# Optimization experiments

Measured on AMD Instinct MI355X. Metric: run time of the kernel, lower is better.

The kernel has to match this reference:

```python
import jax, jax.numpy as jnp
import numpy as np

B, C, T, H, F, KS = 8, 512, 1024, 8, 2048, 3
K = C // H            # head channels = 64
ROPE_D = K // 2       # RoPE rotates half the head channels = 32
EPS = 1e-4


def setup_inputs() -> dict:
    key = jax.random.key(0)
    ks = jax.random.split(key, 12)
    s = 1.0 / np.sqrt(C)
    sf = 1.0 / np.sqrt(F)
    return {
        "x": jax.random.normal(ks[0], (B, C, T), jnp.float32),
        "x_mask": jnp.ones((B, 1, T), jnp.float32),
        "attn_mask": jnp.ones((B, 1, T, T), jnp.float32),
        "wq": jax.random.normal(ks[1], (C, C), jnp.float32) * s,
        "bq": jnp.zeros((C,), jnp.float32),
        "wk": jax.random.normal(ks[2], (C, C), jnp.float32) * s,
        "bk": jnp.zeros((C,), jnp.float32),
        "wv": jax.random.normal(ks[3], (C, C), jnp.float32) * s,
        "bv": jnp.zeros((C,), jnp.float32),
        "wo": jax.random.normal(ks[4], (C, C), jnp.float32) * s,
        "bo": jnp.zeros((C,), jnp.float32),
        "w1": jax.random.normal(ks[5], (F, C, KS), jnp.float32) * s,
        "b1": jnp.zeros((F,), jnp.float32),
        "w2": jax.random.normal(ks[6], (C, F, KS), jnp.float32) * sf,
        "b2": jnp.zeros((C,), jnp.float32),
        "g1": jnp.ones((C,), jnp.float32),
        "be1": jnp.zeros((C,), jnp.float32),
        "g2": jnp.ones((C,), jnp.float32),
        "be2": jnp.zeros((C,), jnp.float32),
    }


def _rope(x):
    # x: (B, H, T, K); rotate first ROPE_D channels, pass the rest through.
    t = x.shape[2]
    theta = 1.0 / (10000.0 ** (jnp.arange(0, ROPE_D, 2, dtype=jnp.float32) / ROPE_D))
    idx = jnp.arange(t, dtype=jnp.float32)[:, None] * theta[None, :]  # (T, d/2)
    idx2 = jnp.concatenate([idx, idx], axis=-1)                       # (T, d)
    cos, sin = jnp.cos(idx2), jnp.sin(idx2)                           # broadcast over B,H
    xr, xp = x[..., :ROPE_D], x[..., ROPE_D:]
    h = ROPE_D // 2
    neg = jnp.concatenate([-xr[..., h:], xr[..., :h]], axis=-1)
    return jnp.concatenate([xr * cos + neg * sin, xp], axis=-1)


def _ln(x, gamma, beta):
    # channel-wise LayerNorm over dim 1 of (B, C, T), eps=1e-4
    mean = jnp.mean(x, axis=1, keepdims=True)
    var = jnp.mean((x - mean) ** 2, axis=1, keepdims=True)
    xn = (x - mean) * jax.lax.rsqrt(var + EPS)
    return xn * gamma[None, :, None] + beta[None, :, None]


def _conv1d(x, w, b):
    # x: (B, Cin, T), w: (Cout, Cin, KS), 'same' padding (KS//2)
    y = jax.lax.conv_general_dilated(
        x, w, window_strides=(1,), padding=[(KS // 2, KS // 2)],
        dimension_numbers=("NCH", "OIH", "NCH"))
    return y + b[None, :, None]


def _forward(x, x_mask, attn_mask, wq, bq, wk, bk, wv, bv, wo, bo,
             w1, b1, w2, b2, g1, be1, g2, be2):
    x = x * x_mask
    # 1x1 conv projections == channel matmuls
    q = jnp.einsum("oc,bct->bot", wq, x) + bq[None, :, None]
    k = jnp.einsum("oc,bct->bot", wk, x) + bk[None, :, None]
    v = jnp.einsum("oc,bct->bot", wv, x) + bv[None, :, None]
    # (B, C, T) -> (B, H, T, K)
    def heads(a):
        return a.reshape(B, H, K, T).transpose(0, 1, 3, 2)
    q, k, v = heads(q), heads(k), heads(v)
    q = _rope(q)
    k = _rope(k)
    scores = jnp.einsum("bhtk,bhsk->bhts", q, k) / jnp.sqrt(jnp.float32(K))
    scores = jnp.where(attn_mask == 0, jnp.float32(-10000.0), scores)
    p = jax.nn.softmax(scores, axis=-1)
    o = jnp.einsum("bhts,bhsk->bhtk", p, v)              # (B,H,T,K)
    o = o.transpose(0, 1, 3, 2).reshape(B, C, T)
    y = jnp.einsum("oc,bct->bot", wo, o) + bo[None, :, None]
    x = _ln(x + y, g1, be1)
    # conv FFN
    h1 = jax.nn.relu(_conv1d(x * x_mask, w1, b1))
    y = _conv1d(h1 * x_mask, w2, b2) * x_mask
    x = _ln(x + y, g2, be2)
    return x


def reference(x, x_mask, attn_mask, wq, bq, wk, bk, wv, bv, wo, bo,
              w1, b1, w2, b2, g1, be1, g2, be2):
    return _forward(x, x_mask, attn_mask, wq, bq, wk, bk, wv, bv, wo, bo,
                    w1, b1, w2, b2, g1, be1, g2, be2)
```

## Files before the change

### kernel.cpp

```cpp
#include <hip/hip_runtime.h>

typedef unsigned short u16;
typedef __attribute__((ext_vector_type(4))) float floatx4;
typedef __attribute__((ext_vector_type(8))) __bf16 bf16x8;
typedef __attribute__((ext_vector_type(4))) unsigned short ushort4v;
typedef __attribute__((ext_vector_type(8))) unsigned short ushort8v;

#define DI __device__ __forceinline__


DI u16 f2bf(float f) {
  union { float f; unsigned u; } v; v.f = f;
  unsigned r = v.u + 0x7fffu + ((v.u >> 16) & 1u);
  return (u16)(r >> 16);
}
DI float bf2f(u16 h) {
  union { unsigned u; float f; } v; v.u = ((unsigned)h) << 16;
  return v.f;
}

#define GLDS(g, l) __builtin_amdgcn_global_load_lds( \
    (const __attribute__((address_space(1))) unsigned int*)(g), \
    (__attribute__((address_space(3))) unsigned int*)(l), 16, 0, 0)

__global__ __launch_bounds__(256, 2) void k_fattn(
    const u16* __restrict__ qb, const u16* __restrict__ kb,
    const u16* __restrict__ vb, const unsigned* __restrict__ mb,
    u16* __restrict__ oT)
{
  __shared__ __align__(16) u16 Ps[4][32 * 64];
  const int tid  = threadIdx.x;
  const int wave = tid >> 6, lane = tid & 63;
  const int lr = lane & 15, kg = lane >> 4;
  const int qt = blockIdx.x, bh = blockIdx.y;
  const int bb = bh >> 3, hh = bh & 7;
  const int wq0 = qt * 128 + wave * 32;
  const float L2E = 1.44269504f;

  const u16* Qp = qb + (size_t)bh * 65536;
  const u16* Kp = kb + (size_t)bh * 65536;
  const u16* Vp = vb + (size_t)bh * 65536;
  u16* Pw = &Ps[wave][0];

  bf16x8 qf[2][2];
#pragma unroll
  for (int i = 0; i < 2; ++i)
#pragma unroll
    for (int h = 0; h < 2; ++h)
      qf[i][h] = *(const bf16x8*)&Qp[(wq0 + i * 16 + lr) * 64 + h * 32 + kg * 8];

  float l_b[2] = {0.f, 0.f};
  floatx4 o_acc[2][4];
#pragma unroll
  for (int i = 0; i < 2; ++i)
#pragma unroll
    for (int j = 0; j < 4; ++j) o_acc[i][j] = (floatx4){0.f, 0.f, 0.f, 0.f};

  bf16x8 kf[4][2], vf[4][2];
#pragma unroll
  for (int a = 0; a < 4; ++a)
#pragma unroll
    for (int h = 0; h < 2; ++h)
      kf[a][h] = *(const bf16x8*)&Kp[(a * 16 + lr) * 64 + h * 32 + kg * 8];

  for (int it = 0; it < 16; ++it) {
    const int s0 = it * 64;
    unsigned mw[2][2];
#pragma unroll
    for (int b = 0; b < 2; ++b) {
      const size_t rw = ((size_t)bb << 15) + ((size_t)(wq0 + b * 16 + lr) << 5) + (s0 >> 5);
      mw[b][0] = mb[rw]; mw[b][1] = mb[rw + 1];
    }
    floatx4 sT[4][2];
    __builtin_amdgcn_s_setprio(1);
#pragma unroll
    for (int a = 0; a < 4; ++a) {
      sT[a][0] = (floatx4){0.f, 0.f, 0.f, 0.f};
      sT[a][1] = (floatx4){0.f, 0.f, 0.f, 0.f};
#pragma unroll
      for (int b = 0; b < 2; ++b)
#pragma unroll
        for (int h = 0; h < 2; ++h)
          sT[a][b] = __builtin_amdgcn_mfma_f32_16x16x32_bf16(kf[a][h], qf[b][h], sT[a][b], 0, 0, 0);
    }
    __builtin_amdgcn_s_setprio(0);
#pragma unroll
    for (int a = 0; a < 4; ++a)
#pragma unroll
      for (int h = 0; h < 2; ++h)
        vf[a][h] = *(const bf16x8*)&Vp[(a * 16 + lr) * 1024 + s0 + h * 32 + kg * 8];
    if (it < 15) {
      const int sn = s0 + 64;
#pragma unroll
      for (int a = 0; a < 4; ++a)
#pragma unroll
        for (int h = 0; h < 2; ++h)
          kf[a][h] = *(const bf16x8*)&Kp[(sn + a * 16 + lr) * 64 + h * 32 + kg * 8];
    }
#pragma unroll
    for (int b = 0; b < 2; ++b) {
      float sum = 0.f;
#pragma unroll
      for (int a = 0; a < 4; ++a)
#pragma unroll
        for (int r = 0; r < 4; ++r) {
          const int sl = a * 16 + kg * 4 + r;
          float sv = sT[a][b][r];
          const unsigned wsel = (sl & 32) ? mw[b][1] : mw[b][0];
          if (!((wsel >> (sl & 31)) & 1u)) sv = -10000.f;
          const float p = exp2f(sv * L2E);
          sT[a][b][r] = p;
          sum += p;
        }
      l_b[b] += sum;
#pragma unroll
      for (int a = 0; a < 4; ++a) {
        ushort4v pk;
#pragma unroll
        for (int r = 0; r < 4; ++r) {
          __bf16 hv = (__bf16)sT[a][b][r];
          pk[r] = *(u16*)&hv;
        }
        const int sl0 = a * 16 + kg * 4;
        *(ushort4v*)&Pw[(b * 16 + lr) * 64 + (sl0 ^ ((lr & 7) << 3))] = pk;
      }
    }
    asm volatile("s_waitcnt lgkmcnt(0)" ::: "memory");
    __builtin_amdgcn_sched_barrier(0);
    bf16x8 pa[2][2];
#pragma unroll
    for (int i = 0; i < 2; ++i)
#pragma unroll
      for (int h = 0; h < 2; ++h)
        pa[i][h] = *(const bf16x8*)&Pw[(i * 16 + lr) * 64 + (((h * 4 + kg) ^ (lr & 7)) << 3)];
    __builtin_amdgcn_s_setprio(1);
#pragma unroll
    for (int jd = 0; jd < 4; ++jd)
#pragma unroll
      for (int i = 0; i < 2; ++i)
#pragma unroll
        for (int h = 0; h < 2; ++h)
          o_acc[i][jd] = __builtin_amdgcn_mfma_f32_16x16x32_bf16(pa[i][h], vf[jd][h], o_acc[i][jd], 0, 0, 0);
    __builtin_amdgcn_s_setprio(0);
  }
#pragma unroll
  for (int i = 0; i < 2; ++i) {
    l_b[i] += __shfl_xor(l_b[i], 16);
    l_b[i] += __shfl_xor(l_b[i], 32);
  }
  float linv[2][4];
#pragma unroll
  for (int i = 0; i < 2; ++i)
#pragma unroll
    for (int r = 0; r < 4; ++r) linv[i][r] = 1.f / __shfl(l_b[i], kg * 4 + r);
#pragma unroll
  for (int i = 0; i < 2; ++i)
#pragma unroll
    for (int jd = 0; jd < 4; ++jd)
#pragma unroll
      for (int r = 0; r < 4; ++r) {
        const int t = wq0 + i * 16 + kg * 4 + r;
        const int c = hh * 64 + jd * 16 + lr;
        oT[((size_t)bb * 1024 + t) * 512 + c] = f2bf(o_acc[i][jd][r] * linv[i][r]);
      }
}

template<int MODE, int BN, int TAPK>
__global__ __launch_bounds__(256) void k_cgemm(
    const u16* __restrict__ A, int lda,
    const u16* __restrict__ Bsrc, int ldb,
    int K,
    u16* __restrict__ o0, u16* __restrict__ o1, u16* __restrict__ o2,
    const float* __restrict__ bias,
    const float* __restrict__ ctab, const float* __restrict__ stab,
    const float* __restrict__ msk)
{
  constexpr int BM = 128;
  constexpr int FN = BN / 32;
  __shared__ __align__(16) u16 As[2 * BM * 32];
  __shared__ __align__(16) u16 Bs[2 * BN * 32];

  const int tid  = threadIdx.x;
  const int wave = tid >> 6, lane = tid & 63;
  const int wm = wave >> 1, wn = wave & 1;
  const int lr = lane & 15, kg = lane >> 4;

  const int nwg = gridDim.x * gridDim.y;
  const int h0  = blockIdx.y * gridDim.x + blockIdx.x;
  const int cpx = nwg >> 3;
  const int tl  = (h0 & 7) * cpx + (h0 >> 3);
  const int bx  = tl % gridDim.x;
  const int by  = tl / gridDim.x;

  const int m0 = bx * BM, n0 = by * BN;
  const int koff = blockIdx.z * K;

  const u16* aP[2][BM / 64];
  const u16* bP[2][BN / 64];
#pragma unroll
  for (int h = 0; h < 2; ++h) {
#pragma unroll
    for (int ch = 0; ch < BM / 64; ++ch) {
      const int idx = ch * 256 + tid;
      const int row = idx >> 2;
      const int kk = (((idx & 3) ^ ((row >> 1) & 3)) << 3);
      aP[h][ch] = A + (size_t)(m0 + row) * lda + koff + h * 32 + kk;
    }
#pragma unroll
    for (int ch = 0; ch < BN / 64; ++ch) {
      const int idx = ch * 256 + tid;
      const int row = idx >> 2;
      const int kk = (((idx & 3) ^ ((row >> 1) & 3)) << 3);
      const int bt = n0 + row;
      size_t rowbase;
      if constexpr (TAPK == 0) {
        rowbase = (size_t)bt * ldb;
      } else {
        const int b = bt >> 10, t = bt & 1023;
        rowbase = ((size_t)(b * 1026 + t)) * TAPK;
      }
      bP[h][ch] = Bsrc + rowbase + koff + h * 32 + kk;
    }
  }

  floatx4 acc[4][FN];
#pragma unroll
  for (int i = 0; i < 4; ++i)
#pragma unroll
    for (int j = 0; j < FN; ++j) acc[i][j] = (floatx4){0.f, 0.f, 0.f, 0.f};

  const int csw = (kg ^ ((lr >> 1) & 3)) * 8;

  for (int k0 = 0; k0 < K; k0 += 64) {
#pragma unroll
    for (int h = 0; h < 2; ++h) {
#pragma unroll
      for (int ch = 0; ch < BM / 64; ++ch)
        GLDS(aP[h][ch] + k0, &As[h * BM * 32 + (ch * 256 + tid) * 8]);
#pragma unroll
      for (int ch = 0; ch < BN / 64; ++ch)
        GLDS(bP[h][ch] + k0, &Bs[h * BN * 32 + (ch * 256 + tid) * 8]);
    }
    __syncthreads();
    bf16x8 af[2][4], bfr[2][FN];
#pragma unroll
    for (int h = 0; h < 2; ++h) {
#pragma unroll
      for (int i = 0; i < 4; ++i)
        af[h][i] = *(const bf16x8*)&As[(h * BM + wm * 64 + i * 16 + lr) * 32 + csw];
#pragma unroll
      for (int j = 0; j < FN; ++j)
        bfr[h][j] = *(const bf16x8*)&Bs[(h * BN + wn * (BN / 2) + j * 16 + lr) * 32 + csw];
    }
#pragma unroll
    for (int h = 0; h < 2; ++h)
#pragma unroll
      for (int i = 0; i < 4; ++i)
#pragma unroll
        for (int j = 0; j < FN; ++j)
          acc[i][j] = __builtin_amdgcn_mfma_f32_16x16x32_bf16(af[h][i], bfr[h][j], acc[i][j], 0, 0, 0);
    __syncthreads();
  }

  const int wrow0 = m0 + wm * 64;
  const int col0  = n0 + wn * (BN / 2);

  if constexpr (MODE == 0) {
    float v[4][FN][4];
#pragma unroll
    for (int i = 0; i < 4; ++i)
#pragma unroll
      for (int j = 0; j < FN; ++j)
#pragma unroll
        for (int r = 0; r < 4; ++r)
          v[i][j][r] = acc[i][j][r] + bias[wrow0 + i * 16 + kg * 4 + r];
    const int sec = wrow0 >> 9;
    const int hh  = (wrow0 & 511) >> 6;
    if (sec < 2) {
      if (sec == 0) {
#pragma unroll
        for (int i = 0; i < 4; ++i)
#pragma unroll
          for (int j = 0; j < FN; ++j)
#pragma unroll
            for (int r = 0; r < 4; ++r) v[i][j][r] *= 0.125f;
      }
#pragma unroll
      for (int j = 0; j < FN; ++j) {
        const int t = (col0 + j * 16 + lr) & 1023;
#pragma unroll
        for (int r = 0; r < 4; ++r) {
          const int a = kg * 4 + r;
          const float cv = ctab[t * 16 + a], sv = stab[t * 16 + a];
          const float a0 = v[0][j][r], a1 = v[1][j][r];
          v[0][j][r] = a0 * cv - a1 * sv;
          v[1][j][r] = a1 * cv + a0 * sv;
        }
      }
      u16* dst = (sec == 0) ? o0 : o1;
#pragma unroll
      for (int i = 0; i < 4; ++i)
#pragma unroll
        for (int j = 0; j < FN; ++j) {
          const int bt = col0 + j * 16 + lr;
          const int b = bt >> 10, t = bt & 1023;
          ushort4v pk;
#pragma unroll
          for (int r = 0; r < 4; ++r) pk[r] = f2bf(v[i][j][r]);
          *(ushort4v*)&dst[(((size_t)b * 8 + hh) * 1024 + t) * 64 + i * 16 + kg * 4] = pk;
        }
    } else {
#pragma unroll
      for (int i = 0; i < 4; ++i)
#pragma unroll
        for (int j = 0; j < FN; ++j) {
          const int bt = col0 + j * 16 + lr;
          const int b = bt >> 10, t = bt & 1023;
#pragma unroll
          for (int r = 0; r < 4; ++r) {
            const int dk = i * 16 + kg * 4 + r;
            o2[(((size_t)b * 8 + hh) * 64 + dk) * 1024 + t] = f2bf(v[i][j][r]);
          }
        }
    }
  } else if constexpr (MODE == 3) {
#pragma unroll
    for (int i = 0; i < 4; ++i)
#pragma unroll
      for (int j = 0; j < FN; ++j) {
        const int bt = col0 + j * 16 + lr;
        const int c0 = wrow0 + i * 16 + kg * 4;
        ushort4v pk;
#pragma unroll
        for (int r = 0; r < 4; ++r) pk[r] = f2bf(acc[i][j][r] + bias[c0 + r]);
        *(ushort4v*)&o0[(size_t)bt * 512 + c0] = pk;
      }
  } else if constexpr (MODE == 4) {
#pragma unroll
    for (int i = 0; i < 4; ++i) {
      const int r0 = wrow0 + i * 16 + kg * 4;
#pragma unroll
      for (int j = 0; j < FN; ++j) {
        const int bt = col0 + j * 16 + lr;
        const int b = bt >> 10, t = bt & 1023;
        const float mv = msk[(size_t)b * 1024 + t];
        ushort4v pk;
#pragma unroll
        for (int r = 0; r < 4; ++r)
          pk[r] = f2bf(fmaxf(acc[i][j][r] + bias[r0 + r], 0.f) * mv);
        *(ushort4v*)&o0[((size_t)(b * 1026 + t + 1)) * 2048 + r0] = pk;
      }
    }
  } else {
    u16* dst = o0 + (size_t)blockIdx.z * 8 * 1024 * 512;
    const bool z0 = (blockIdx.z == 0);
#pragma unroll
    for (int i = 0; i < 4; ++i)
#pragma unroll
      for (int j = 0; j < FN; ++j) {
        const int bt = col0 + j * 16 + lr;
        const int b = bt >> 10, t = bt & 1023;
        const int c0 = wrow0 + i * 16 + kg * 4;
        const float mv = msk[(size_t)b * 1024 + t];
        ushort4v pk;
#pragma unroll
        for (int r = 0; r < 4; ++r) {
          const float bv = z0 ? bias[c0 + r] : 0.f;
          pk[r] = f2bf((acc[i][j][r] + bv) * mv);
        }
        *(ushort4v*)&dst[(size_t)bt * 512 + c0] = pk;
      }
  }
}

__global__ __launch_bounds__(256) void k_prep(
    const float* __restrict__ wq, const float* __restrict__ wk,
    const float* __restrict__ wv, const float* __restrict__ wo,
    const float* __restrict__ w1, const float* __restrict__ w2,
    const float* __restrict__ bq, const float* __restrict__ bk,
    const float* __restrict__ bv, const float* __restrict__ am,
    u16* __restrict__ wqkv, u16* __restrict__ wob,
    u16* __restrict__ w1p, u16* __restrict__ w2p,
    float* __restrict__ bqkv, float* __restrict__ ctab, float* __restrict__ stab,
    unsigned* __restrict__ mbits, u16* __restrict__ x2p, u16* __restrict__ h1p)
{
  const int bid = blockIdx.x;
  if (bid < 4096) {
    const int seg = bid >> 10;
    const int i = (bid & 1023) * 256 + threadIdx.x;
    const float* src = (seg == 0) ? wq : (seg == 1) ? wk : (seg == 2) ? wv : wo;
    u16* dst = (seg < 3) ? (wqkv + (size_t)seg * 512 * 512) : wob;
    dst[i] = f2bf(src[i]);
  } else if (bid < 16384) {
    const int i = (bid - 4096) * 256 + threadIdx.x;
    const int f = i / 1536, rem = i % 1536;
    const int kk = rem >> 9, c = rem & 511;
    w1p[i] = f2bf(w1[f * 1536 + c * 3 + kk]);
  } else if (bid < 28672) {
    const int i = (bid - 16384) * 256 + threadIdx.x;
    const int c = i / 6144, rem = i % 6144;
    const int kk = rem >> 11, f = rem & 2047;
    w2p[i] = f2bf(w2[c * 6144 + f * 3 + kk]);
  } else if (bid < 29696) {
    const int i = (bid - 28672) * 256 + threadIdx.x;
    const float* src = am + (size_t)i * 32;
    unsigned w = 0;
#pragma unroll
    for (int q = 0; q < 32; ++q) w |= (src[q] != 0.f) ? (1u << q) : 0u;
    mbits[i] = w;
  } else if (bid < 29760) {
    const int i = (bid - 29696) * 256 + threadIdx.x;
    const int t = i >> 4, a = i & 15;
    const float theta = powf(10000.f, -(float)a / 16.f);
    const float ang = (float)t * theta;
    ctab[i] = cosf(ang);
    stab[i] = sinf(ang);
  } else if (bid == 29760) {
    for (int i = threadIdx.x; i < 1536; i += 256)
      bqkv[i] = (i < 512) ? bq[i] : (i < 1024) ? bk[i - 512] : bv[i - 1024];
  } else {
    int zb = bid - 29761;
    if (zb < 16) {
      const int b = zb >> 1;
      const size_t row = (zb & 1) ? 1025 : 0;
      u16* r = x2p + ((size_t)b * 1026 + row) * 512;
      for (int i = threadIdx.x; i < 512; i += 256) r[i] = 0;
    } else {
      zb -= 16;
      const int b = zb >> 1;
      const size_t row = (zb & 1) ? 1025 : 0;
      u16* r = h1p + ((size_t)b * 1026 + row) * 2048;
      for (int i = threadIdx.x; i < 2048; i += 256) r[i] = 0;
    }
  }
}

__global__ __launch_bounds__(256) void k_tcvt(const float* __restrict__ in, u16* __restrict__ out,
                                              const float* __restrict__ msk, int R, int TT) {
  __shared__ u16 tile[64][65];
  const int b = blockIdx.z;
  const int r0 = blockIdx.x * 64, t0 = blockIdx.y * 64;
  const int tx = threadIdx.x & 63, ty = threadIdx.x >> 6;
  const float mv = msk ? msk[(size_t)b * TT + t0 + tx] : 1.f;
  const float* ib = in + (size_t)b * R * TT;
#pragma unroll
  for (int rr = ty; rr < 64; rr += 4)
    tile[rr][tx] = f2bf(ib[(size_t)(r0 + rr) * TT + t0 + tx] * mv);
  __syncthreads();
  u16* ob = out + (size_t)b * TT * R;
#pragma unroll
  for (int tt = ty; tt < 64; tt += 4)
    ob[(size_t)(t0 + tt) * R + r0 + tx] = tile[tx][tt];
}

__global__ __launch_bounds__(256) void k_ln1(
    const u16* __restrict__ xbT, const u16* __restrict__ y1T,
    const float* __restrict__ xm, const float* __restrict__ g,
    const float* __restrict__ be, u16* __restrict__ x2T, u16* __restrict__ x2p)
{
  const int lane = threadIdx.x & 63, wv = threadIdx.x >> 6;
  const int row = blockIdx.x * 4 + wv;
  const int b = row >> 10, t = row & 1023;
  const size_t base = (size_t)row * 512 + lane * 8;
  ushort8v ux = *(const ushort8v*)&xbT[base];
  ushort8v uy = *(const ushort8v*)&y1T[base];
  float v[8];
  float sum = 0.f, ss = 0.f;
#pragma unroll
  for (int q = 0; q < 8; ++q) {
    v[q] = bf2f(ux[q]) + bf2f(uy[q]);
    sum += v[q]; ss += v[q] * v[q];
  }
#pragma unroll
  for (int o = 32; o; o >>= 1) { sum += __shfl_xor(sum, o); ss += __shfl_xor(ss, o); }
  const float mean = sum * (1.f / 512.f);
  const float var  = ss * (1.f / 512.f) - mean * mean;
  const float rs   = rsqrtf(var + 1e-4f);
  const float m    = xm[(size_t)b * 1024 + t];
  ushort8v on, om;
#pragma unroll
  for (int q = 0; q < 8; ++q) {
    const int c = lane * 8 + q;
    const float nv = (v[q] - mean) * rs * g[c] + be[c];
    on[q] = f2bf(nv);
    om[q] = f2bf(nv * m);
  }
  *(ushort8v*)&x2T[base] = on;
  *(ushort8v*)&x2p[((size_t)(b * 1026 + t + 1)) * 512 + lane * 8] = om;
}

__global__ __launch_bounds__(256) void k_ln2_stats(
    const u16* __restrict__ x2T, const u16* __restrict__ c2p,
    float2* __restrict__ mr)
{
  constexpr size_t S = (size_t)8 * 1024 * 512;
  const int lane = threadIdx.x & 63, wv = threadIdx.x >> 6;
  const int row = blockIdx.x * 4 + wv;
  const size_t base = (size_t)row * 512 + lane * 8;
  ushort8v u0 = *(const ushort8v*)&x2T[base];
  ushort8v u1 = *(const ushort8v*)&c2p[base];
  ushort8v u2 = *(const ushort8v*)&c2p[S + base];
  float sum = 0.f, ss = 0.f;
#pragma unroll
  for (int q = 0; q < 8; ++q) {
    const float v = bf2f(u0[q]) + bf2f(u1[q]) + bf2f(u2[q]);
    sum += v; ss += v * v;
  }
#pragma unroll
  for (int o = 32; o; o >>= 1) { sum += __shfl_xor(sum, o); ss += __shfl_xor(ss, o); }
  if (lane == 0) {
    const float mean = sum * (1.f / 512.f);
    const float var  = ss * (1.f / 512.f) - mean * mean;
    mr[row] = (float2){mean, rsqrtf(var + 1e-4f)};
  }
}

__global__ __launch_bounds__(256) void k_ln2_write(
    const u16* __restrict__ x2T, const u16* __restrict__ c2p,
    const float2* __restrict__ mr,
    const float* __restrict__ g, const float* __restrict__ be,
    float* __restrict__ out)
{
  constexpr size_t S = (size_t)8 * 1024 * 512;
  __shared__ float tile[64][65];
  const int cc0 = blockIdx.x * 64, t0 = blockIdx.y * 64, b = blockIdx.z;
  const int tid = threadIdx.x;
  const int c4 = (tid & 15) * 4;
  const int tr = tid >> 4;
  float g4[4], b4[4];
#pragma unroll
  for (int q = 0; q < 4; ++q) { g4[q] = g[cc0 + c4 + q]; b4[q] = be[cc0 + c4 + q]; }
#pragma unroll
  for (int it = 0; it < 4; ++it) {
    const int tt = tr + it * 16;
    const int row = b * 1024 + t0 + tt;
    const size_t base = (size_t)row * 512 + cc0 + c4;
    ushort4v u0 = *(const ushort4v*)&x2T[base];
    ushort4v u1 = *(const ushort4v*)&c2p[base];
    ushort4v u2 = *(const ushort4v*)&c2p[S + base];
    const float2 s = mr[row];
#pragma unroll
    for (int q = 0; q < 4; ++q) {
      const float v = bf2f(u0[q]) + bf2f(u1[q]) + bf2f(u2[q]);
      tile[tt][c4 + q] = (v - s.x) * s.y * g4[q] + b4[q];
    }
  }
  __syncthreads();
  const int tx = tid & 63, cg = tid >> 6;
#pragma unroll
  for (int c = cg; c < 64; c += 4)
    out[((size_t)b * 512 + cc0 + c) * 1024 + t0 + tx] = tile[tx][c];
}

extern "C" void kernel_launch(void* const* d_in, const int* in_sizes, int n_in,
                              void* d_out, int out_size, void* d_ws, size_t ws_size,
                              hipStream_t stream) {
  (void)in_sizes; (void)n_in; (void)out_size; (void)ws_size;
  const float* x   = (const float*)d_in[0];
  const float* xm  = (const float*)d_in[1];
  const float* am  = (const float*)d_in[2];
  const float* wq  = (const float*)d_in[3];
  const float* bq  = (const float*)d_in[4];
  const float* wk  = (const float*)d_in[5];
  const float* bk  = (const float*)d_in[6];
  const float* wv  = (const float*)d_in[7];
  const float* bv  = (const float*)d_in[8];
  const float* wo  = (const float*)d_in[9];
  const float* bo  = (const float*)d_in[10];
  const float* w1  = (const float*)d_in[11];
  const float* b1  = (const float*)d_in[12];
  const float* w2  = (const float*)d_in[13];
  const float* b2  = (const float*)d_in[14];
  const float* g1  = (const float*)d_in[15];
  const float* be1 = (const float*)d_in[16];
  const float* g2  = (const float*)d_in[17];
  const float* be2 = (const float*)d_in[18];
  float* out = (float*)d_out;

  char* ws = (char*)d_ws;
  size_t off = 0;
  auto alloc = [&](size_t bytes) { char* p = ws + off; off += (bytes + 255) & ~(size_t)255; return p; };

  u16*   wqkv = (u16*)  alloc((size_t)1536 * 512 * 2);
  u16*   wob  = (u16*)  alloc((size_t)512 * 512 * 2);
  u16*   w1p  = (u16*)  alloc((size_t)2048 * 1536 * 2);
  u16*   w2p  = (u16*)  alloc((size_t)512 * 6144 * 2);
  float* bqkv = (float*)alloc(1536 * 4);
  float* ctab = (float*)alloc(1024 * 16 * 4);
  float* stab = (float*)alloc(1024 * 16 * 4);
  unsigned* mbits = (unsigned*)alloc((size_t)8 * 1024 * 32 * 4);
  float2* mr  = (float2*)alloc((size_t)8192 * 8);
  u16*   x2T  = (u16*)  alloc((size_t)8 * 1024 * 512 * 2);
  u16*   x2p  = (u16*)  alloc((size_t)8 * 1026 * 512 * 2);
  u16*   h1p  = (u16*)  alloc((size_t)8 * 1026 * 2048 * 2);
  u16*   y1T  = (u16*)  alloc((size_t)8 * 1024 * 512 * 2);
  u16*   xbT  = (u16*)  alloc((size_t)8 * 1024 * 512 * 2);
  u16*   oT   = (u16*)  alloc((size_t)8 * 1024 * 512 * 2);
  u16*   qkv3 = (u16*)  alloc((size_t)3 * 8 * 8 * 1024 * 64 * 2);
  u16*   c2p  = (u16*)  alloc((size_t)2 * 8 * 1024 * 512 * 2);

  u16* qb = qkv3;
  u16* kb = qkv3 + (size_t)8 * 8 * 1024 * 64;
  u16* vb = kb   + (size_t)8 * 8 * 1024 * 64;

  dim3 blk(256);

  k_prep<<<dim3(29793), blk, 0, stream>>>(
      wq, wk, wv, wo, w1, w2, bq, bk, bv, am,
      wqkv, wob, w1p, w2p, bqkv, ctab, stab, mbits, x2p, h1p);

  k_tcvt<<<dim3(8, 16, 8), blk, 0, stream>>>(x, xbT, xm, 512, 1024);

  k_cgemm<0, 128, 0><<<dim3(12, 64), blk, 0, stream>>>(
      wqkv, 512, xbT, 512, 512, qb, kb, vb, bqkv, ctab, stab, nullptr);

  k_fattn<<<dim3(8, 64), blk, 0, stream>>>(qb, kb, vb, mbits, oT);

  k_cgemm<3, 64, 0><<<dim3(4, 128), blk, 0, stream>>>(
      wob, 512, oT, 512, 512, y1T, nullptr, nullptr, bo, nullptr, nullptr, nullptr);

  k_ln1<<<dim3(2048), blk, 0, stream>>>(xbT, y1T, xm, g1, be1, x2T, x2p);

  k_cgemm<4, 128, 512><<<dim3(16, 64), blk, 0, stream>>>(
      w1p, 1536, x2p, 0, 1536, h1p, nullptr, nullptr, b1, nullptr, nullptr, xm);
  k_cgemm<5, 64, 2048><<<dim3(4, 128, 2), blk, 0, stream>>>(
      w2p, 6144, h1p, 0, 3072, c2p, nullptr, nullptr, b2, nullptr, nullptr, xm);

  k_ln2_stats<<<dim3(2048), blk, 0, stream>>>(x2T, c2p, mr);
  k_ln2_write<<<dim3(8, 16, 8), blk, 0, stream>>>(x2T, c2p, mr, g2, be2, out);
}
```

Baseline: 299.6 us.

## Fuse input transpose into prep kernel, vectorize conv weight repack, prefetch mask bits

The x transpose/convert kernel is merged into k_prep as extra blocks, removing one launch and letting it overlap with the weight conversion. The conv weight repack now has each thread handle all three taps, which cuts the block count and reads the source contiguously. In attention, the mask bitwords for the next tile are loaded one iteration early alongside the K prefetch, hiding their latency. The cost is a shared-memory tile declared in every k_prep block, plus extra registers in the attention loop.

```diff
diff --git a/kernel.cpp b/kernel.cpp
--- a/kernel.cpp
+++ b/kernel.cpp
@@ -63,14 +63,15 @@
     for (int h = 0; h < 2; ++h)
       kf[a][h] = *(const bf16x8*)&Kp[(a * 16 + lr) * 64 + h * 32 + kg * 8];
 
+  unsigned mw[2][2];
+#pragma unroll
+  for (int b = 0; b < 2; ++b) {
+    const size_t rw = ((size_t)bb << 15) + ((size_t)(wq0 + b * 16 + lr) << 5);
+    mw[b][0] = mb[rw]; mw[b][1] = mb[rw + 1];
+  }
+
   for (int it = 0; it < 16; ++it) {
     const int s0 = it * 64;
-    unsigned mw[2][2];
-#pragma unroll
-    for (int b = 0; b < 2; ++b) {
-      const size_t rw = ((size_t)bb << 15) + ((size_t)(wq0 + b * 16 + lr) << 5) + (s0 >> 5);
-      mw[b][0] = mb[rw]; mw[b][1] = mb[rw + 1];
-    }
     floatx4 sT[4][2];
     __builtin_amdgcn_s_setprio(1);
 #pragma unroll
@@ -89,6 +90,7 @@
 #pragma unroll
       for (int h = 0; h < 2; ++h)
         vf[a][h] = *(const bf16x8*)&Vp[(a * 16 + lr) * 1024 + s0 + h * 32 + kg * 8];
+    unsigned mwn[2][2];
     if (it < 15) {
       const int sn = s0 + 64;
 #pragma unroll
@@ -96,6 +98,11 @@
 #pragma unroll
         for (int h = 0; h < 2; ++h)
           kf[a][h] = *(const bf16x8*)&Kp[(sn + a * 16 + lr) * 64 + h * 32 + kg * 8];
+#pragma unroll
+      for (int b = 0; b < 2; ++b) {
+        const size_t rw = ((size_t)bb << 15) + ((size_t)(wq0 + b * 16 + lr) << 5) + (sn >> 5);
+        mwn[b][0] = mb[rw]; mwn[b][1] = mb[rw + 1];
+      }
     }
 #pragma unroll
     for (int b = 0; b < 2; ++b) {
@@ -124,6 +131,10 @@
         const int sl0 = a * 16 + kg * 4;
         *(ushort4v*)&Pw[(b * 16 + lr) * 64 + (sl0 ^ ((lr & 7) << 3))] = pk;
       }
+    }
+    if (it < 15) {
+#pragma unroll
+      for (int b = 0; b < 2; ++b) { mw[b][0] = mwn[b][0]; mw[b][1] = mwn[b][1]; }
     }
     asm volatile("s_waitcnt lgkmcnt(0)" ::: "memory");
     __builtin_amdgcn_sched_barrier(0);
@@ -379,11 +390,14 @@
     const float* __restrict__ w1, const float* __restrict__ w2,
     const float* __restrict__ bq, const float* __restrict__ bk,
     const float* __restrict__ bv, const float* __restrict__ am,
+    const float* __restrict__ x, const float* __restrict__ xm,
     u16* __restrict__ wqkv, u16* __restrict__ wob,
     u16* __restrict__ w1p, u16* __restrict__ w2p,
     float* __restrict__ bqkv, float* __restrict__ ctab, float* __restrict__ stab,
-    unsigned* __restrict__ mbits, u16* __restrict__ x2p, u16* __restrict__ h1p)
+    unsigned* __restrict__ mbits, u16* __restrict__ x2p, u16* __restrict__ h1p,
+    u16* __restrict__ xbT)
 {
+  __shared__ u16 tile[64][65];
   const int bid = blockIdx.x;
   if (bid < 4096) {
     const int seg = bid >> 10;
@@ -391,35 +405,39 @@
     const float* src = (seg == 0) ? wq : (seg == 1) ? wk : (seg == 2) ? wv : wo;
     u16* dst = (seg < 3) ? (wqkv + (size_t)seg * 512 * 512) : wob;
     dst[i] = f2bf(src[i]);
-  } else if (bid < 16384) {
+  } else if (bid < 8192) {
     const int i = (bid - 4096) * 256 + threadIdx.x;
-    const int f = i / 1536, rem = i % 1536;
-    const int kk = rem >> 9, c = rem & 511;
-    w1p[i] = f2bf(w1[f * 1536 + c * 3 + kk]);
-  } else if (bid < 28672) {
-    const int i = (bid - 16384) * 256 + threadIdx.x;
-    const int c = i / 6144, rem = i % 6144;
-    const int kk = rem >> 11, f = rem & 2047;
-    w2p[i] = f2bf(w2[c * 6144 + f * 3 + kk]);
-  } else if (bid < 29696) {
-    const int i = (bid - 28672) * 256 + threadIdx.x;
+    const int f = i >> 9, c = i & 511;
+    const float* s = &w1[(size_t)f * 1536 + c * 3];
+#pragma unroll
+    for (int kk = 0; kk < 3; ++kk)
+      w1p[(size_t)f * 1536 + kk * 512 + c] = f2bf(s[kk]);
+  } else if (bid < 12288) {
+    const int i = (bid - 8192) * 256 + threadIdx.x;
+    const int c = i >> 11, f = i & 2047;
+    const float* s = &w2[(size_t)c * 6144 + f * 3];
+#pragma unroll
+    for (int kk = 0; kk < 3; ++kk)
+      w2p[(size_t)c * 6144 + kk * 2048 + f] = f2bf(s[kk]);
+  } else if (bid < 13312) {
+    const int i = (bid - 12288) * 256 + threadIdx.x;
     const float* src = am + (size_t)i * 32;
     unsigned w = 0;
 #pragma unroll
     for (int q = 0; q < 32; ++q) w |= (src[q] != 0.f) ? (1u << q) : 0u;
     mbits[i] = w;
-  } else if (bid < 29760) {
-    const int i = (bid - 29696) * 256 + threadIdx.x;
+  } else if (bid < 13376) {
+    const int i = (bid - 13312) * 256 + threadIdx.x;
     const int t = i >> 4, a = i & 15;
     const float theta = powf(10000.f, -(float)a / 16.f);
     const float ang = (float)t * theta;
     ctab[i] = cosf(ang);
     stab[i] = sinf(ang);
-  } else if (bid == 29760) {
+  } else if (bid == 13376) {
     for (int i = threadIdx.x; i < 1536; i += 256)
       bqkv[i] = (i < 512) ? bq[i] : (i < 1024) ? bk[i - 512] : bv[i - 1024];
-  } else {
-    int zb = bid - 29761;
+  } else if (bid < 13409) {
+    int zb = bid - 13377;
     if (zb < 16) {
       const int b = zb >> 1;
       const size_t row = (zb & 1) ? 1025 : 0;
@@ -432,25 +450,22 @@
       u16* r = h1p + ((size_t)b * 1026 + row) * 2048;
       for (int i = threadIdx.x; i < 2048; i += 256) r[i] = 0;
     }
-  }
-}
-
-__global__ __launch_bounds__(256) void k_tcvt(const float* __restrict__ in, u16* __restrict__ out,
-                                              const float* __restrict__ msk, int R, int TT) {
-  __shared__ u16 tile[64][65];
-  const int b = blockIdx.z;
-  const int r0 = blockIdx.x * 64, t0 = blockIdx.y * 64;
-  const int tx = threadIdx.x & 63, ty = threadIdx.x >> 6;
-  const float mv = msk ? msk[(size_t)b * TT + t0 + tx] : 1.f;
-  const float* ib = in + (size_t)b * R * TT;
-#pragma unroll
-  for (int rr = ty; rr < 64; rr += 4)
-    tile[rr][tx] = f2bf(ib[(size_t)(r0 + rr) * TT + t0 + tx] * mv);
-  __syncthreads();
-  u16* ob = out + (size_t)b * TT * R;
-#pragma unroll
-  for (int tt = ty; tt < 64; tt += 4)
-    ob[(size_t)(t0 + tt) * R + r0 + tx] = tile[tx][tt];
+  } else {
+    const int zb = bid - 13409;
+    const int b = zb & 7, tt0 = (zb >> 3) & 15, rr0 = zb >> 7;
+    const int r0 = rr0 * 64, t0 = tt0 * 64;
+    const int tx = threadIdx.x & 63, ty = threadIdx.x >> 6;
+    const float mv = xm[(size_t)b * 1024 + t0 + tx];
+    const float* ib = x + (size_t)b * 512 * 1024;
+#pragma unroll
+    for (int rr = ty; rr < 64; rr += 4)
+      tile[rr][tx] = f2bf(ib[(size_t)(r0 + rr) * 1024 + t0 + tx] * mv);
+    __syncthreads();
+    u16* ob = xbT + (size_t)b * 1024 * 512;
+#pragma unroll
+    for (int t2 = ty; t2 < 64; t2 += 4)
+      ob[(size_t)(t0 + t2) * 512 + r0 + tx] = tile[tx][t2];
+  }
 }
 
 __global__ __launch_bounds__(256) void k_ln1(
@@ -605,11 +620,9 @@
 
   dim3 blk(256);
 
-  k_prep<<<dim3(29793), blk, 0, stream>>>(
-      wq, wk, wv, wo, w1, w2, bq, bk, bv, am,
-      wqkv, wob, w1p, w2p, bqkv, ctab, stab, mbits, x2p, h1p);
-
-  k_tcvt<<<dim3(8, 16, 8), blk, 0, stream>>>(x, xbT, xm, 512, 1024);
+  k_prep<<<dim3(14433), blk, 0, stream>>>(
+      wq, wk, wv, wo, w1, w2, bq, bk, bv, am, x, xm,
+      wqkv, wob, w1p, w2p, bqkv, ctab, stab, mbits, x2p, h1p, xbT);
 
   k_cgemm<0, 128, 0><<<dim3(12, 64), blk, 0, stream>>>(
       wqkv, 512, xbT, 512, 512, qb, kb, vb, bqkv, ctab, stab, nullptr);
```

New measurement: 290.8 us (median of 2 runs). 1.03x faster.
